# Optimization experiments

Hardware: AMD Instinct MI355X
Metric: run time of the kernel (lower is better)

## Reference

```python
import jax, jax.numpy as jnp
import numpy as np

EMBED = 256
HEADS = 8
LEVELS = 4
POINTS = 4
HD = EMBED // HEADS  # 32
SHAPES = [(100, 100), (50, 50), (25, 25), (13, 13)]  # (H, W) per level
NV = sum(h * w for h, w in SHAPES)  # 13294
BS = 2


def _lin_params(k, fan_in, fan_out):
    s = 1.0 / np.sqrt(fan_in)
    kw, kb = jax.random.split(k)
    W = jax.random.uniform(kw, (fan_in, fan_out), jnp.float32, -s, s)
    b = jax.random.uniform(kb, (fan_out,), jnp.float32, -s, s)
    return W, b


def setup_inputs():
    key = jax.random.key(0)
    ks = jax.random.split(key, 10)
    inp = {
        "query": jax.random.normal(ks[0], (BS, NV, EMBED), jnp.float32),
        "key": jax.random.normal(ks[1], (BS, NV, EMBED), jnp.float32),
        "value": jax.random.normal(ks[2], (BS, NV, EMBED), jnp.float32),
        "query_pos": jax.random.normal(ks[3], (BS, NV, EMBED), jnp.float32),
        "reference_points": jax.random.uniform(ks[4], (BS, NV, LEVELS, 2), jnp.float32),
        "spatial_shapes": jnp.array(SHAPES, jnp.int32),
        "level_start_index": jnp.array(np.cumsum([0] + [h * w for h, w in SHAPES[:-1]]), jnp.int32),
        "key_padding_mask": jnp.zeros((BS, NV), bool),
    }
    inp["W_value"], inp["b_value"] = _lin_params(ks[5], EMBED, EMBED)
    inp["W_off"], inp["b_off"] = _lin_params(ks[6], EMBED, HEADS * LEVELS * POINTS * 2)
    inp["W_attn"], inp["b_attn"] = _lin_params(ks[7], EMBED, HEADS * LEVELS * POINTS)
    inp["W_out"], inp["b_out"] = _lin_params(ks[8], EMBED, EMBED)
    inp["W_ffn"], inp["b_ffn"] = _lin_params(ks[9], EMBED, EMBED)
    return inp


def _bilinear(v, x, y, H, W):
    # v: (bs, heads, H*W, hd); x, y: (bs, heads, n) pixel coords (align_corners=False)
    # zero padding outside the feature map (matches torch grid_sample padding_mode='zeros')
    x0 = jnp.floor(x)
    y0 = jnp.floor(y)
    lx = x - x0
    ly = y - y0
    x0 = x0.astype(jnp.int32)
    y0 = y0.astype(jnp.int32)

    def g(xi, yi):
        valid = ((xi >= 0) & (xi < W) & (yi >= 0) & (yi < H)).astype(v.dtype)
        idx = jnp.clip(yi, 0, H - 1) * W + jnp.clip(xi, 0, W - 1)
        return jnp.take_along_axis(v, idx[..., None], axis=2) * valid[..., None]

    return (g(x0, y0) * ((1 - lx) * (1 - ly))[..., None]
            + g(x0 + 1, y0) * (lx * (1 - ly))[..., None]
            + g(x0, y0 + 1) * ((1 - lx) * ly)[..., None]
            + g(x0 + 1, y0 + 1) * (lx * ly)[..., None])


def _forward(query, key, value, query_pos, reference_points, shapes, starts,
             key_padding_mask, W_value, b_value, W_off, b_off, W_attn, b_attn,
             W_out, b_out, W_ffn, b_ffn):
    bs, nq, _ = query.shape
    identity = query  # residual taken BEFORE adding positional encoding (mmcv semantics)
    q = query + query_pos
    v = value @ W_value + b_value
    v = jnp.where(key_padding_mask[..., None], 0.0, v).reshape(bs, -1, HEADS, HD)
    off = (q @ W_off + b_off).reshape(bs, nq, HEADS, LEVELS, POINTS, 2)
    aw = jax.nn.softmax((q @ W_attn + b_attn).reshape(bs, nq, HEADS, LEVELS * POINTS), axis=-1)
    aw = aw.reshape(bs, nq, HEADS, LEVELS, POINTS)
    # offset normalizer is (W, H) per level
    wh = jnp.array([[w, h] for h, w in shapes], jnp.float32)
    loc = reference_points[:, :, None, :, None, :] + off / wh[None, None, None, :, None, :]
    out = jnp.zeros((bs, HEADS, nq, HD), q.dtype)
    for l, (H, W) in enumerate(shapes):
        s = starts[l]
        vl = v[:, s:s + H * W].transpose(0, 2, 1, 3)  # (bs, heads, H*W, hd)
        x = (loc[:, :, :, l, :, 0] * W - 0.5).transpose(0, 2, 1, 3).reshape(bs, HEADS, nq * POINTS)
        y = (loc[:, :, :, l, :, 1] * H - 0.5).transpose(0, 2, 1, 3).reshape(bs, HEADS, nq * POINTS)
        smp = _bilinear(vl, x, y, H, W).reshape(bs, HEADS, nq, POINTS, HD)
        wl = aw[:, :, :, l].transpose(0, 2, 1, 3)  # (bs, heads, nq, P)
        out = out + jnp.sum(smp * wl[..., None], axis=3)
    out = out.transpose(0, 2, 1, 3).reshape(bs, nq, EMBED)
    out = out @ W_out + b_out + identity
    return out @ W_ffn + b_ffn


def reference(query, key, value, query_pos, reference_points, spatial_shapes,
              level_start_index, key_padding_mask, W_value, b_value, W_off, b_off,
              W_attn, b_attn, W_out, b_out, W_ffn, b_ffn):
    # spatial shapes / level starts are structural metadata -> treat as static ints
    shapes = [tuple(int(x) for x in r) for r in np.asarray(spatial_shapes)]
    starts = [int(x) for x in np.asarray(level_start_index)]
    return _forward(query, key, value, query_pos, reference_points, shapes, starts,
                    key_padding_mask, W_value, b_value, W_off, b_off, W_attn, b_attn,
                    W_out, b_out, W_ffn, b_ffn)
```

## Files before the change

### kernel.cpp

```cpp
#include <hip/hip_runtime.h>
#include <hip/hip_bf16.h>
#include <math.h>

#define NQ 13294
#define NV 13294
#define M_ROWS (2*NQ)
#define MP 26624

typedef __attribute__((ext_vector_type(8))) short bf16x8;
typedef __attribute__((ext_vector_type(4))) float f32x4;
typedef __attribute__((ext_vector_type(2))) float f32x2;

__device__ __forceinline__ float4 ld4(const float* p){ return *(const float4*)p; }
__device__ __forceinline__ float bfu_lo(unsigned int u){ return __uint_as_float(u << 16); }
__device__ __forceinline__ float bfu_hi(unsigned int u){ return __uint_as_float(u & 0xffff0000u); }
__device__ __forceinline__ unsigned short f2bf(float f){
  unsigned int u = __float_as_uint(f);
  u += 0x7fffu + ((u >> 16) & 1u);
  return (unsigned short)(u >> 16);
}
__device__ __forceinline__ unsigned int pk2(float a, float b){
  return (unsigned int)f2bf(a) | ((unsigned int)f2bf(b) << 16);
}
__device__ __forceinline__ void gl_lds16(const unsigned short* g, unsigned short* l) {
  __builtin_amdgcn_global_load_lds(
      (const __attribute__((address_space(1))) unsigned int*)g,
      (__attribute__((address_space(3))) unsigned int*)l, 16, 0, 0);
}

__global__ __launch_bounds__(256) void prep_all(
    const float* __restrict__ value, const float* __restrict__ query,
    const float* __restrict__ qpos,
    unsigned short* __restrict__ val_bf, unsigned short* __restrict__ q_bf,
    unsigned short* __restrict__ q2_bf,
    const float* __restrict__ wv, const float* __restrict__ wo,
    const float* __restrict__ wa, const float* __restrict__ wu,
    const float* __restrict__ wf, unsigned short* __restrict__ wt,
    float* __restrict__ bias_c,
    const float* __restrict__ b_out, const float* __restrict__ b_ffn)
{
  if (blockIdx.x >= 2048) {
    const int n = threadIdx.x;
    float acc = b_ffn[n];
    #pragma unroll 8
    for (int k = 0; k < 256; ++k)
      acc = fmaf(b_out[k], wf[k * 256 + n], acc);
    bias_c[n] = acc;
    return;
  }

  const int total = MP * 64;
  for (int i = blockIdx.x * 256 + threadIdx.x; i < total; i += 2048 * 256) {
    const int e = i * 4;
    ushort4 a = make_ushort4(0,0,0,0), b = make_ushort4(0,0,0,0), c = make_ushort4(0,0,0,0);
    if (e < M_ROWS * 256) {
      float4 v4 = ld4(value + e);
      a = make_ushort4(f2bf(v4.x), f2bf(v4.y), f2bf(v4.z), f2bf(v4.w));
      float4 q4 = ld4(query + e);
      float4 p4 = ld4(qpos + e);
      b = make_ushort4(f2bf(q4.x+p4.x), f2bf(q4.y+p4.y), f2bf(q4.z+p4.z), f2bf(q4.w+p4.w));
      c = make_ushort4(f2bf(q4.x), f2bf(q4.y), f2bf(q4.z), f2bf(q4.w));
    }
    *(ushort4*)(val_bf + e) = a;
    *(ushort4*)(q_bf   + e) = b;
    *(ushort4*)(q2_bf  + e) = c;
  }
  for (int t = blockIdx.x * 256 + threadIdx.x; t < 294912; t += 2048 * 256) {
    if (t < 229376) {
      const float* src; int Nn; int base;
      if      (t < 65536)  { src = wv; Nn = 256; base = 0; }
      else if (t < 131072) { src = wo; Nn = 256; base = 65536; }
      else if (t < 163840) { src = wa; Nn = 128; base = 131072; }
      else                 { src = wf; Nn = 256; base = 163840; }
      const int local = t - base;
      const int n = local >> 8, k = local & 255;
      wt[t] = f2bf(src[k * Nn + n]);
    } else {
      const int local = t - 229376;
      wt[t] = f2bf(wu[local]);
    }
  }
}

__global__ __launch_bounds__(256) void gemm_voa2(
    const unsigned short* __restrict__ val_bf, const unsigned short* __restrict__ q_bf,
    const unsigned short* __restrict__ wv_t, const unsigned short* __restrict__ woa_t,
    const unsigned short* __restrict__ wf_t, const unsigned short* __restrict__ wu_bf,
    const float* __restrict__ b_value, const float* __restrict__ b_off,
    const float* __restrict__ b_attn,
    unsigned char* __restrict__ vbuf8, unsigned short* __restrict__ oa,
    unsigned short* __restrict__ wof_t)
{
  __shared__ unsigned short lds[32768];

  const int bx = blockIdx.x;
  const int mode = (bx < 1664) ? 0 : (bx < 4160) ? 1 : 2;
  const int lin  = (mode == 0) ? bx : (mode == 1) ? bx - 1664 : bx - 4160;
  const int nwg  = (mode == 0) ? 1664 : (mode == 1) ? 2496 : 16;
  const int ncol = (mode == 0) ? 4 : (mode == 1) ? 6 : 4;
  const unsigned short* A  = (mode == 0) ? val_bf : (mode == 1) ? q_bf : wf_t;
  const unsigned short* Bt = (mode == 0) ? wv_t : (mode == 1) ? woa_t : wu_bf;

  const int swz  = (lin & 7) * (nwg >> 3) + (lin >> 3);
  const int brow = (swz / ncol) * 64;
  const int bcol = (swz % ncol) * 64;

  const int tid  = threadIdx.x;
  const int wid  = tid >> 6, lane = tid & 63;
  const int wr   = wid >> 1, wc = wid & 1;
  const int fr   = lane & 15, fg = lane >> 4;

  {
    const int r0   = lane >> 3;
    const int slot = lane & 7;
    #pragma unroll
    for (int t = 0; t < 4; ++t) {
      #pragma unroll
      for (int c = 0; c < 2; ++c) {
        const int row = (wid * 2 + c) * 8 + r0;
        const int gsl = slot ^ (row & 7);
        gl_lds16(A  + (size_t)(brow + row) * 256 + t * 64 + (gsl << 3),
                 &lds[t * 4096 + (wid * 2 + c) * 512]);
        gl_lds16(Bt + (size_t)(bcol + row) * 256 + t * 64 + (gsl << 3),
                 &lds[16384 + t * 4096 + (wid * 2 + c) * 512]);
      }
    }
  }
  __syncthreads();

  f32x4 acc[2][2];
  #pragma unroll
  for (int m = 0; m < 2; ++m)
    #pragma unroll
    for (int n = 0; n < 2; ++n)
      acc[m][n] = (f32x4){0.f, 0.f, 0.f, 0.f};

  #pragma unroll
  for (int t = 0; t < 4; ++t) {
    const char* as = (const char*)&lds[t * 4096];
    const char* bs = (const char*)&lds[16384 + t * 4096];
    #pragma unroll
    for (int kk = 0; kk < 2; ++kk) {
      const int kb = kk * 64 + fg * 16;
      bf16x8 af[2], bfv[2];
      #pragma unroll
      for (int m = 0; m < 2; ++m) {
        const int r = wr * 32 + m * 16 + fr;
        af[m] = *(const bf16x8*)(as + r * 128 + (kb ^ ((r & 7) << 4)));
      }
      #pragma unroll
      for (int n = 0; n < 2; ++n) {
        const int r = wc * 32 + n * 16 + fr;
        bfv[n] = *(const bf16x8*)(bs + r * 128 + (kb ^ ((r & 7) << 4)));
      }
      #pragma unroll
      for (int m = 0; m < 2; ++m)
        #pragma unroll
        for (int n = 0; n < 2; ++n)
          acc[m][n] = __builtin_amdgcn_mfma_f32_16x16x32_bf16(af[m], bfv[n], acc[m][n], 0, 0, 0);
    }
  }

  __syncthreads();
  float* csh = (float*)lds;
  const int c0 = bcol + wc * 32 + fr;
  const int c1 = c0 + 16;
  float bn0 = 0.f, bn1 = 0.f;
  if (mode == 0) { bn0 = b_value[c0]; bn1 = b_value[c1]; }
  else if (mode == 1) {
    bn0 = (c0 < 256) ? b_off[c0] : b_attn[c0 - 256];
    bn1 = (c1 < 256) ? b_off[c1] : b_attn[c1 - 256];
  }
  #pragma unroll
  for (int m = 0; m < 2; ++m)
    #pragma unroll
    for (int j = 0; j < 4; ++j) {
      const int row = wr * 32 + m * 16 + fg * 4 + j;
      csh[row * 64 + wc * 32 + fr]      = acc[m][0][j] + bn0;
      csh[row * 64 + wc * 32 + 16 + fr] = acc[m][1][j] + bn1;
    }
  __syncthreads();
  #pragma unroll
  for (int i = 0; i < 4; ++i) {
    const int rl = i * 16 + (tid >> 4);
    const int gr = brow + rl;
    if (gr >= M_ROWS) continue;
    const int c4 = (tid & 15) * 4;
    float4 v = *(const float4*)&csh[rl * 64 + c4];
    if (mode == 0) {
      const int head = (bcol + c4) >> 5;
      const int ch   = c4 & 31;
      int r = 0;
      r = __builtin_amdgcn_cvt_pk_fp8_f32(v.x, v.y, r, 0);
      r = __builtin_amdgcn_cvt_pk_fp8_f32(v.z, v.w, r, 1);
      *(int*)&vbuf8[((size_t)head * M_ROWS + gr) * 32 + ch] = r;
    } else if (mode == 1) {
      ushort4 pk = make_ushort4(f2bf(v.x), f2bf(v.y), f2bf(v.z), f2bf(v.w));
      *(ushort4*)&oa[(size_t)gr * 384 + bcol + c4] = pk;
    } else {
      ushort4 pk = make_ushort4(f2bf(v.x), f2bf(v.y), f2bf(v.z), f2bf(v.w));
      *(ushort4*)&wof_t[(size_t)gr * 256 + bcol + c4] = pk;
    }
  }
}

__global__ __launch_bounds__(256) void gemm_final(
    const unsigned short* __restrict__ A1, const unsigned short* __restrict__ B1,
    const unsigned short* __restrict__ A2, const unsigned short* __restrict__ B2,
    const float* __restrict__ bias_c, float* __restrict__ C)
{
  __shared__ unsigned short lds[32768];

  const int nwg = 1664;
  const int lin = blockIdx.x;
  const int swz = (lin & 7) * (nwg >> 3) + (lin >> 3);
  const int brow = (swz >> 2) * 64;
  const int bcol = (swz & 3) * 64;

  const int tid  = threadIdx.x;
  const int wid  = tid >> 6, lane = tid & 63;
  const int wr   = wid >> 1, wc = wid & 1;
  const int fr   = lane & 15, fg = lane >> 4;

  auto stage = [&](const unsigned short* A, const unsigned short* Bt) {
    const int r0   = lane >> 3;
    const int slot = lane & 7;
    #pragma unroll
    for (int t = 0; t < 4; ++t) {
      #pragma unroll
      for (int c = 0; c < 2; ++c) {
        const int row = (wid * 2 + c) * 8 + r0;
        const int gsl = slot ^ (row & 7);
        gl_lds16(A  + (size_t)(brow + row) * 256 + t * 64 + (gsl << 3),
                 &lds[t * 4096 + (wid * 2 + c) * 512]);
        gl_lds16(Bt + (size_t)(bcol + row) * 256 + t * 64 + (gsl << 3),
                 &lds[16384 + t * 4096 + (wid * 2 + c) * 512]);
      }
    }
  };

  f32x4 acc[2][2];
  #pragma unroll
  for (int m = 0; m < 2; ++m)
    #pragma unroll
    for (int n = 0; n < 2; ++n)
      acc[m][n] = (f32x4){0.f, 0.f, 0.f, 0.f};

  auto compute = [&]() {
    #pragma unroll
    for (int t = 0; t < 4; ++t) {
      const char* as = (const char*)&lds[t * 4096];
      const char* bs = (const char*)&lds[16384 + t * 4096];
      #pragma unroll
      for (int kk = 0; kk < 2; ++kk) {
        const int kb = kk * 64 + fg * 16;
        bf16x8 af[2], bfv[2];
        #pragma unroll
        for (int m = 0; m < 2; ++m) {
          const int r = wr * 32 + m * 16 + fr;
          af[m] = *(const bf16x8*)(as + r * 128 + (kb ^ ((r & 7) << 4)));
        }
        #pragma unroll
        for (int n = 0; n < 2; ++n) {
          const int r = wc * 32 + n * 16 + fr;
          bfv[n] = *(const bf16x8*)(bs + r * 128 + (kb ^ ((r & 7) << 4)));
        }
        #pragma unroll
        for (int m = 0; m < 2; ++m)
          #pragma unroll
          for (int n = 0; n < 2; ++n)
            acc[m][n] = __builtin_amdgcn_mfma_f32_16x16x32_bf16(af[m], bfv[n], acc[m][n], 0, 0, 0);
      }
    }
  };

  stage(A1, B1);
  __syncthreads();
  compute();
  __syncthreads();
  stage(A2, B2);
  __syncthreads();
  compute();

  __syncthreads();
  float* csh = (float*)lds;
  const int c0 = bcol + wc * 32 + fr;
  const int c1 = c0 + 16;
  const float bn0 = bias_c[c0];
  const float bn1 = bias_c[c1];
  #pragma unroll
  for (int m = 0; m < 2; ++m)
    #pragma unroll
    for (int j = 0; j < 4; ++j) {
      const int row = wr * 32 + m * 16 + fg * 4 + j;
      csh[row * 64 + wc * 32 + fr]      = acc[m][0][j] + bn0;
      csh[row * 64 + wc * 32 + 16 + fr] = acc[m][1][j] + bn1;
    }
  __syncthreads();
  #pragma unroll
  for (int i = 0; i < 4; ++i) {
    const int rl = i * 16 + (tid >> 4);
    const int gr = brow + rl;
    if (gr >= M_ROWS) continue;
    const int c4 = (tid & 15) * 4;
    *(float4*)&C[(size_t)gr * 256 + bcol + c4] = *(const float4*)&csh[rl * 64 + c4];
  }
}

__global__ __launch_bounds__(256) void msda7(
    const unsigned char* __restrict__ v, const unsigned short* __restrict__ oa,
    const float* __restrict__ ref, unsigned short* __restrict__ attout)
{
  constexpr int LW[4] = {100, 50, 25, 13};
  constexpr int LS[4] = {0, 10000, 12500, 13125};

  __shared__ int2   sidx[64][17];
  __shared__ float4 swt [64][17];

  const int bid   = blockIdx.x;
  const int h     = bid & 7;
  const int chunk = bid >> 3;
  const int tid   = threadIdx.x;
  const int q     = tid >> 2;
  const int c     = tid & 3;
  const int bq    = chunk * 64 + q;
  const bool active = bq < M_ROWS;
  const int b     = (bq >= NQ) ? 1 : 0;

  if (active) {
    const int l = c;
    const int W = LW[l];
    const float fD = (float)W;
    const unsigned short* oarow = oa + (size_t)bq * 384;

    uint2 lg = *(const uint2*)(oarow + 256 + h * 16 + l * 4);
    float g0 = bfu_lo(lg.x), g1 = bfu_hi(lg.x), g2 = bfu_lo(lg.y), g3 = bfu_hi(lg.y);
    float mx = fmaxf(fmaxf(g0, g1), fmaxf(g2, g3));
    mx = fmaxf(mx, __shfl_xor(mx, 1));
    mx = fmaxf(mx, __shfl_xor(mx, 2));
    float e0 = __expf(g0-mx), e1 = __expf(g1-mx), e2 = __expf(g2-mx), e3 = __expf(g3-mx);
    float s = e0 + e1 + e2 + e3;
    s += __shfl_xor(s, 1);
    s += __shfl_xor(s, 2);
    const float inv = 1.f / s;
    const float ee[4] = {e0*inv, e1*inv, e2*inv, e3*inv};

    uint4 ov = *(const uint4*)(oarow + h * 32 + l * 8);
    const float oxy[8] = {bfu_lo(ov.x), bfu_hi(ov.x), bfu_lo(ov.y), bfu_hi(ov.y),
                          bfu_lo(ov.z), bfu_hi(ov.z), bfu_lo(ov.w), bfu_hi(ov.w)};
    const float rx = ref[(size_t)bq * 8 + l * 2];
    const float ry = ref[(size_t)bq * 8 + l * 2 + 1];
    const int rowbase = b * NV + LS[l];

    #pragma unroll
    for (int j = 0; j < 4; ++j) {
      const float x = fmaf(rx, fD, oxy[2*j])   - 0.5f;
      const float y = fmaf(ry, fD, oxy[2*j+1]) - 0.5f;
      const float x0f = floorf(x), y0f = floorf(y);
      const float lx = x - x0f, ly = y - y0f;
      const int x0 = (int)x0f, y0 = (int)y0f;
      const int y1 = y0 + 1;
      const int xbase = min(max(x0, 0), W - 2);
      const float wx0 = 1.f - lx, wx1 = lx;
      const float we0 = (x0 == xbase     ? wx0 : 0.f) + (x0 == xbase - 1 ? wx1 : 0.f);
      const float we1 = (x0 == xbase + 1 ? wx0 : 0.f) + (x0 == xbase     ? wx1 : 0.f);
      const int cy0 = min(max(y0, 0), W - 1), cy1 = min(max(y1, 0), W - 1);
      const float wy0 = (y0 >= 0 && y0 < W) ? (1.f - ly) : 0.f;
      const float wy1 = (y1 >= 0 && y1 < W) ? ly : 0.f;
      const float wt = ee[j];
      const int p = l * 4 + j;
      sidx[q][p] = make_int2((rowbase + cy0 * W + xbase) * 32,
                             (rowbase + cy1 * W + xbase) * 32);
      swt[q][p] = make_float4(wt * wy0 * we0, wt * wy0 * we1,
                              wt * wy1 * we0, wt * wy1 * we1);
    }
  }
  __syncthreads();

  if (active) {
    const unsigned char* vb = v + (size_t)h * M_ROWS * 32 + c * 16;
    const int el = c >> 1;
    f32x2 acc2[8];
    #pragma unroll
    for (int k = 0; k < 8; ++k) acc2[k] = (f32x2){0.f, 0.f};
    #pragma unroll
    for (int p = 0; p < 16; ++p) {
      const int2   ix = sidx[q][p];
      const float4 w4 = swt[q][p];
      uint4 r0 = *(const uint4*)(vb + ix.x);
      uint4 r1 = *(const uint4*)(vb + ix.y);
      const float wa = el ? w4.y : w4.x;
      const float wb = el ? w4.w : w4.z;
      const f32x2 wav = (f32x2){wa, wa};
      const f32x2 wbv = (f32x2){wb, wb};
      acc2[0] = wav * __builtin_amdgcn_cvt_pk_f32_fp8(r0.x, 0) + acc2[0];
      acc2[1] = wav * __builtin_amdgcn_cvt_pk_f32_fp8(r0.x, 1) + acc2[1];
      acc2[2] = wav * __builtin_amdgcn_cvt_pk_f32_fp8(r0.y, 0) + acc2[2];
      acc2[3] = wav * __builtin_amdgcn_cvt_pk_f32_fp8(r0.y, 1) + acc2[3];
      acc2[4] = wav * __builtin_amdgcn_cvt_pk_f32_fp8(r0.z, 0) + acc2[4];
      acc2[5] = wav * __builtin_amdgcn_cvt_pk_f32_fp8(r0.z, 1) + acc2[5];
      acc2[6] = wav * __builtin_amdgcn_cvt_pk_f32_fp8(r0.w, 0) + acc2[6];
      acc2[7] = wav * __builtin_amdgcn_cvt_pk_f32_fp8(r0.w, 1) + acc2[7];
      acc2[0] = wbv * __builtin_amdgcn_cvt_pk_f32_fp8(r1.x, 0) + acc2[0];
      acc2[1] = wbv * __builtin_amdgcn_cvt_pk_f32_fp8(r1.x, 1) + acc2[1];
      acc2[2] = wbv * __builtin_amdgcn_cvt_pk_f32_fp8(r1.y, 0) + acc2[2];
      acc2[3] = wbv * __builtin_amdgcn_cvt_pk_f32_fp8(r1.y, 1) + acc2[3];
      acc2[4] = wbv * __builtin_amdgcn_cvt_pk_f32_fp8(r1.z, 0) + acc2[4];
      acc2[5] = wbv * __builtin_amdgcn_cvt_pk_f32_fp8(r1.z, 1) + acc2[5];
      acc2[6] = wbv * __builtin_amdgcn_cvt_pk_f32_fp8(r1.w, 0) + acc2[6];
      acc2[7] = wbv * __builtin_amdgcn_cvt_pk_f32_fp8(r1.w, 1) + acc2[7];
    }
    #pragma unroll
    for (int k = 0; k < 8; ++k) {
      acc2[k][0] += __shfl_xor(acc2[k][0], 2);
      acc2[k][1] += __shfl_xor(acc2[k][1], 2);
    }
    if (c < 2) {
      uint4 pkA, pkB;
      pkA.x = pk2(acc2[0][0], acc2[0][1]);
      pkA.y = pk2(acc2[1][0], acc2[1][1]);
      pkA.z = pk2(acc2[2][0], acc2[2][1]);
      pkA.w = pk2(acc2[3][0], acc2[3][1]);
      pkB.x = pk2(acc2[4][0], acc2[4][1]);
      pkB.y = pk2(acc2[5][0], acc2[5][1]);
      pkB.z = pk2(acc2[6][0], acc2[6][1]);
      pkB.w = pk2(acc2[7][0], acc2[7][1]);
      unsigned short* dst = attout + (size_t)bq * 256 + h * 32 + c * 16;
      *(uint4*)dst = pkA;
      *(uint4*)(dst + 8) = pkB;
    }
  }
}

extern "C" void kernel_launch(void* const* d_in, const int* in_sizes, int n_in,
                              void* d_out, int out_size, void* d_ws, size_t ws_size,
                              hipStream_t stream) {
  const float* query  = (const float*)d_in[0];
  const float* value  = (const float*)d_in[2];
  const float* qpos   = (const float*)d_in[3];
  const float* refpts = (const float*)d_in[4];
  const float* W_value = (const float*)d_in[8];
  const float* b_value = (const float*)d_in[9];
  const float* W_off   = (const float*)d_in[10];
  const float* b_off   = (const float*)d_in[11];
  const float* W_attn  = (const float*)d_in[12];
  const float* b_attn  = (const float*)d_in[13];
  const float* W_out   = (const float*)d_in[14];
  const float* b_out   = (const float*)d_in[15];
  const float* W_ffn   = (const float*)d_in[16];
  const float* b_ffn   = (const float*)d_in[17];
  float* out = (float*)d_out;

  unsigned short* oa    = (unsigned short*)d_ws;
  unsigned char*  vbuf8 = (unsigned char*)(oa + (size_t)MP * 384);
  unsigned short* AB1   = (unsigned short*)(vbuf8 + (size_t)8 * M_ROWS * 32);
  unsigned short* QB    = AB1 + (size_t)MP * 256;
  unsigned short* Q2B   = QB + (size_t)MP * 256;
  unsigned short* wts   = Q2B + (size_t)MP * 256;
  unsigned short* wv_t  = wts;
  unsigned short* woa_t = wts + 65536;
  unsigned short* wf_t  = wts + 163840;
  unsigned short* wu_bf = wts + 229376;
  unsigned short* wof_t = wts + 294912;
  float*          bias_c = (float*)(wof_t + 65536);

  const dim3 blk(256);

  prep_all<<<dim3(2049), blk, 0, stream>>>(value, query, qpos, AB1, QB, Q2B,
      W_value, W_off, W_attn, W_out, W_ffn, wts, bias_c, b_out, b_ffn);

  gemm_voa2<<<dim3(1664 + 2496 + 16), blk, 0, stream>>>(
      AB1, QB, wv_t, woa_t, wf_t, wu_bf, b_value, b_off, b_attn, vbuf8, oa, wof_t);

  msda7<<<dim3(8 * 416), blk, 0, stream>>>(vbuf8, oa, refpts, AB1);

  gemm_final<<<dim3(1664), blk, 0, stream>>>(AB1, wof_t, Q2B, wf_t, bias_c, out);
}
```

Baseline: 109.5 us.

## Fuse fp32-to-bf16 activation conversion into GEMM LDS staging, drop prep pass

Removes the pass that converted value, query and query+pos to bf16 copies in workspace. The GEMMs now stage fp32 rows straight into LDS and convert them to bf16 while building the MFMA fragments. The query+pos input is handled as two accumulated passes (query, then qpos) using linearity, and the final GEMM reads fp32 query directly. The weight prep shrinks to a small kernel. This cuts the write and re-read of three bf16 activation copies, at the cost of twice the LDS traffic per A tile, extra pack instructions, doubled MFMA work for the offset/attention GEMM, and separate bf16 rounding of query and pos.

```diff
diff --git a/kernel.cpp b/kernel.cpp
--- a/kernel.cpp
+++ b/kernel.cpp
@@ -11,7 +11,6 @@
 typedef __attribute__((ext_vector_type(4))) float f32x4;
 typedef __attribute__((ext_vector_type(2))) float f32x2;
 
-__device__ __forceinline__ float4 ld4(const float* p){ return *(const float4*)p; }
 __device__ __forceinline__ float bfu_lo(unsigned int u){ return __uint_as_float(u << 16); }
 __device__ __forceinline__ float bfu_hi(unsigned int u){ return __uint_as_float(u & 0xffff0000u); }
 __device__ __forceinline__ unsigned short f2bf(float f){
@@ -22,68 +21,48 @@
 __device__ __forceinline__ unsigned int pk2(float a, float b){
   return (unsigned int)f2bf(a) | ((unsigned int)f2bf(b) << 16);
 }
-__device__ __forceinline__ void gl_lds16(const unsigned short* g, unsigned short* l) {
+__device__ __forceinline__ void gl_lds16(const void* g, unsigned short* l) {
   __builtin_amdgcn_global_load_lds(
       (const __attribute__((address_space(1))) unsigned int*)g,
       (__attribute__((address_space(3))) unsigned int*)l, 16, 0, 0);
 }
 
-__global__ __launch_bounds__(256) void prep_all(
-    const float* __restrict__ value, const float* __restrict__ query,
-    const float* __restrict__ qpos,
-    unsigned short* __restrict__ val_bf, unsigned short* __restrict__ q_bf,
-    unsigned short* __restrict__ q2_bf,
+__global__ __launch_bounds__(256) void prep_w(
     const float* __restrict__ wv, const float* __restrict__ wo,
     const float* __restrict__ wa, const float* __restrict__ wu,
     const float* __restrict__ wf, unsigned short* __restrict__ wt,
     float* __restrict__ bias_c,
     const float* __restrict__ b_out, const float* __restrict__ b_ffn)
 {
-  if (blockIdx.x >= 2048) {
+  const int bx = blockIdx.x;
+  if (bx < 64) {
+    for (int t = bx * 256 + threadIdx.x; t < 294912; t += 64 * 256) {
+      if (t < 229376) {
+        const float* src; int Nn; int base;
+        if      (t < 65536)  { src = wv; Nn = 256; base = 0; }
+        else if (t < 131072) { src = wo; Nn = 256; base = 65536; }
+        else if (t < 163840) { src = wa; Nn = 128; base = 131072; }
+        else                 { src = wf; Nn = 256; base = 163840; }
+        const int local = t - base;
+        const int n = local >> 8, k = local & 255;
+        wt[t] = f2bf(src[k * Nn + n]);
+      } else {
+        wt[t] = f2bf(wu[t - 229376]);
+      }
+    }
+  } else {
     const int n = threadIdx.x;
     float acc = b_ffn[n];
     #pragma unroll 8
     for (int k = 0; k < 256; ++k)
       acc = fmaf(b_out[k], wf[k * 256 + n], acc);
     bias_c[n] = acc;
-    return;
-  }
-
-  const int total = MP * 64;
-  for (int i = blockIdx.x * 256 + threadIdx.x; i < total; i += 2048 * 256) {
-    const int e = i * 4;
-    ushort4 a = make_ushort4(0,0,0,0), b = make_ushort4(0,0,0,0), c = make_ushort4(0,0,0,0);
-    if (e < M_ROWS * 256) {
-      float4 v4 = ld4(value + e);
-      a = make_ushort4(f2bf(v4.x), f2bf(v4.y), f2bf(v4.z), f2bf(v4.w));
-      float4 q4 = ld4(query + e);
-      float4 p4 = ld4(qpos + e);
-      b = make_ushort4(f2bf(q4.x+p4.x), f2bf(q4.y+p4.y), f2bf(q4.z+p4.z), f2bf(q4.w+p4.w));
-      c = make_ushort4(f2bf(q4.x), f2bf(q4.y), f2bf(q4.z), f2bf(q4.w));
-    }
-    *(ushort4*)(val_bf + e) = a;
-    *(ushort4*)(q_bf   + e) = b;
-    *(ushort4*)(q2_bf  + e) = c;
-  }
-  for (int t = blockIdx.x * 256 + threadIdx.x; t < 294912; t += 2048 * 256) {
-    if (t < 229376) {
-      const float* src; int Nn; int base;
-      if      (t < 65536)  { src = wv; Nn = 256; base = 0; }
-      else if (t < 131072) { src = wo; Nn = 256; base = 65536; }
-      else if (t < 163840) { src = wa; Nn = 128; base = 131072; }
-      else                 { src = wf; Nn = 256; base = 163840; }
-      const int local = t - base;
-      const int n = local >> 8, k = local & 255;
-      wt[t] = f2bf(src[k * Nn + n]);
-    } else {
-      const int local = t - 229376;
-      wt[t] = f2bf(wu[local]);
-    }
-  }
-}
-
-__global__ __launch_bounds__(256) void gemm_voa2(
-    const unsigned short* __restrict__ val_bf, const unsigned short* __restrict__ q_bf,
+  }
+}
+
+__global__ __launch_bounds__(256) void gemm_voa3(
+    const float* __restrict__ value, const float* __restrict__ query,
+    const float* __restrict__ qpos,
     const unsigned short* __restrict__ wv_t, const unsigned short* __restrict__ woa_t,
     const unsigned short* __restrict__ wf_t, const unsigned short* __restrict__ wu_bf,
     const float* __restrict__ b_value, const float* __restrict__ b_off,
@@ -98,7 +77,6 @@
   const int lin  = (mode == 0) ? bx : (mode == 1) ? bx - 1664 : bx - 4160;
   const int nwg  = (mode == 0) ? 1664 : (mode == 1) ? 2496 : 16;
   const int ncol = (mode == 0) ? 4 : (mode == 1) ? 6 : 4;
-  const unsigned short* A  = (mode == 0) ? val_bf : (mode == 1) ? q_bf : wf_t;
   const unsigned short* Bt = (mode == 0) ? wv_t : (mode == 1) ? woa_t : wu_bf;
 
   const int swz  = (lin & 7) * (nwg >> 3) + (lin >> 3);
@@ -111,22 +89,17 @@
   const int fr   = lane & 15, fg = lane >> 4;
 
   {
-    const int r0   = lane >> 3;
-    const int slot = lane & 7;
-    #pragma unroll
-    for (int t = 0; t < 4; ++t) {
+    const int r0 = lane >> 3, slot = lane & 7;
+    #pragma unroll
+    for (int t = 0; t < 4; ++t)
       #pragma unroll
       for (int c = 0; c < 2; ++c) {
         const int row = (wid * 2 + c) * 8 + r0;
         const int gsl = slot ^ (row & 7);
-        gl_lds16(A  + (size_t)(brow + row) * 256 + t * 64 + (gsl << 3),
-                 &lds[t * 4096 + (wid * 2 + c) * 512]);
         gl_lds16(Bt + (size_t)(bcol + row) * 256 + t * 64 + (gsl << 3),
                  &lds[16384 + t * 4096 + (wid * 2 + c) * 512]);
       }
-    }
-  }
-  __syncthreads();
+  }
 
   f32x4 acc[2][2];
   #pragma unroll
@@ -135,29 +108,103 @@
     for (int n = 0; n < 2; ++n)
       acc[m][n] = (f32x4){0.f, 0.f, 0.f, 0.f};
 
-  #pragma unroll
-  for (int t = 0; t < 4; ++t) {
-    const char* as = (const char*)&lds[t * 4096];
-    const char* bs = (const char*)&lds[16384 + t * 4096];
-    #pragma unroll
-    for (int kk = 0; kk < 2; ++kk) {
-      const int kb = kk * 64 + fg * 16;
-      bf16x8 af[2], bfv[2];
-      #pragma unroll
-      for (int m = 0; m < 2; ++m) {
-        const int r = wr * 32 + m * 16 + fr;
-        af[m] = *(const bf16x8*)(as + r * 128 + (kb ^ ((r & 7) << 4)));
-      }
-      #pragma unroll
-      for (int n = 0; n < 2; ++n) {
-        const int r = wc * 32 + n * 16 + fr;
-        bfv[n] = *(const bf16x8*)(bs + r * 128 + (kb ^ ((r & 7) << 4)));
-      }
-      #pragma unroll
-      for (int m = 0; m < 2; ++m)
-        #pragma unroll
-        for (int n = 0; n < 2; ++n)
-          acc[m][n] = __builtin_amdgcn_mfma_f32_16x16x32_bf16(af[m], bfv[n], acc[m][n], 0, 0, 0);
+  if (mode == 2) {
+    {
+      const int r0 = lane >> 3, slot = lane & 7;
+      #pragma unroll
+      for (int t = 0; t < 4; ++t)
+        #pragma unroll
+        for (int c = 0; c < 2; ++c) {
+          const int row = (wid * 2 + c) * 8 + r0;
+          const int gsl = slot ^ (row & 7);
+          gl_lds16(wf_t + (size_t)(brow + row) * 256 + t * 64 + (gsl << 3),
+                   &lds[t * 4096 + (wid * 2 + c) * 512]);
+        }
+    }
+    __syncthreads();
+    #pragma unroll
+    for (int t = 0; t < 4; ++t) {
+      const char* as = (const char*)&lds[t * 4096];
+      const char* bs = (const char*)&lds[16384 + t * 4096];
+      #pragma unroll
+      for (int kk = 0; kk < 2; ++kk) {
+        const int kb = kk * 64 + fg * 16;
+        bf16x8 af[2], bfv[2];
+        #pragma unroll
+        for (int m = 0; m < 2; ++m) {
+          const int r = wr * 32 + m * 16 + fr;
+          af[m] = *(const bf16x8*)(as + r * 128 + (kb ^ ((r & 7) << 4)));
+        }
+        #pragma unroll
+        for (int n = 0; n < 2; ++n) {
+          const int r = wc * 32 + n * 16 + fr;
+          bfv[n] = *(const bf16x8*)(bs + r * 128 + (kb ^ ((r & 7) << 4)));
+        }
+        #pragma unroll
+        for (int m = 0; m < 2; ++m)
+          #pragma unroll
+          for (int n = 0; n < 2; ++n)
+            acc[m][n] = __builtin_amdgcn_mfma_f32_16x16x32_bf16(af[m], bfv[n], acc[m][n], 0, 0, 0);
+      }
+    }
+  } else {
+    const int npass = (mode == 0) ? 1 : 2;
+    for (int ps = 0; ps < npass; ++ps) {
+      const float* S = (mode == 0) ? value : (ps == 0 ? query : qpos);
+      for (int half = 0; half < 2; ++half) {
+        if (ps | half) __syncthreads();
+        {
+          const int rl = lane >> 4;
+          const int sl = lane & 15;
+          #pragma unroll
+          for (int t2 = 0; t2 < 2; ++t2) {
+            const int kt = half * 2 + t2;
+            #pragma unroll
+            for (int i = 0; i < 4; ++i) {
+              const int c = wid * 4 + i;
+              const int row = c * 4 + rl;
+              const int gr = min(brow + row, M_ROWS - 1);
+              const int gsl = sl ^ (row & 7);
+              gl_lds16(S + (size_t)gr * 256 + kt * 64 + gsl * 4,
+                       &lds[t2 * 8192 + c * 512]);
+            }
+          }
+        }
+        __syncthreads();
+        #pragma unroll
+        for (int t2 = 0; t2 < 2; ++t2) {
+          const int kt = half * 2 + t2;
+          const char* as = (const char*)&lds[t2 * 8192];
+          const char* bs = (const char*)&lds[16384 + kt * 4096];
+          #pragma unroll
+          for (int kk = 0; kk < 2; ++kk) {
+            const int s  = kk * 8 + fg * 2;
+            const int kb = kk * 64 + fg * 16;
+            bf16x8 af[2], bfv[2];
+            #pragma unroll
+            for (int m = 0; m < 2; ++m) {
+              const int r  = wr * 32 + m * 16 + fr;
+              const int e7 = r & 7;
+              f32x4 a0 = *(const f32x4*)(as + r * 256 + ((s       ^ e7) << 4));
+              f32x4 a1 = *(const f32x4*)(as + r * 256 + (((s + 1) ^ e7) << 4));
+              union { unsigned int u[4]; bf16x8 h; } cv;
+              cv.u[0] = pk2(a0[0], a0[1]); cv.u[1] = pk2(a0[2], a0[3]);
+              cv.u[2] = pk2(a1[0], a1[1]); cv.u[3] = pk2(a1[2], a1[3]);
+              af[m] = cv.h;
+            }
+            #pragma unroll
+            for (int n = 0; n < 2; ++n) {
+              const int r = wc * 32 + n * 16 + fr;
+              bfv[n] = *(const bf16x8*)(bs + r * 128 + (kb ^ ((r & 7) << 4)));
+            }
+            #pragma unroll
+            for (int m = 0; m < 2; ++m)
+              #pragma unroll
+              for (int n = 0; n < 2; ++n)
+                acc[m][n] = __builtin_amdgcn_mfma_f32_16x16x32_bf16(af[m], bfv[n], acc[m][n], 0, 0, 0);
+          }
+        }
+      }
     }
   }
 
@@ -184,7 +231,7 @@
   for (int i = 0; i < 4; ++i) {
     const int rl = i * 16 + (tid >> 4);
     const int gr = brow + rl;
-    if (gr >= M_ROWS) continue;
+    if (gr >= M_ROWS && mode != 2) continue;
     const int c4 = (tid & 15) * 4;
     float4 v = *(const float4*)&csh[rl * 64 + c4];
     if (mode == 0) {
@@ -204,9 +251,9 @@
   }
 }
 
-__global__ __launch_bounds__(256) void gemm_final(
-    const unsigned short* __restrict__ A1, const unsigned short* __restrict__ B1,
-    const unsigned short* __restrict__ A2, const unsigned short* __restrict__ B2,
+__global__ __launch_bounds__(256) void gemm_final2(
+    const unsigned short* __restrict__ attout, const unsigned short* __restrict__ wof_t,
+    const float* __restrict__ query, const unsigned short* __restrict__ wf_t,
     const float* __restrict__ bias_c, float* __restrict__ C)
 {
   __shared__ unsigned short lds[32768];
@@ -222,21 +269,17 @@
   const int wr   = wid >> 1, wc = wid & 1;
   const int fr   = lane & 15, fg = lane >> 4;
 
-  auto stage = [&](const unsigned short* A, const unsigned short* Bt) {
-    const int r0   = lane >> 3;
-    const int slot = lane & 7;
-    #pragma unroll
-    for (int t = 0; t < 4; ++t) {
+  auto stage_b = [&](const unsigned short* Bt) {
+    const int r0 = lane >> 3, slot = lane & 7;
+    #pragma unroll
+    for (int t = 0; t < 4; ++t)
       #pragma unroll
       for (int c = 0; c < 2; ++c) {
         const int row = (wid * 2 + c) * 8 + r0;
         const int gsl = slot ^ (row & 7);
-        gl_lds16(A  + (size_t)(brow + row) * 256 + t * 64 + (gsl << 3),
-                 &lds[t * 4096 + (wid * 2 + c) * 512]);
         gl_lds16(Bt + (size_t)(bcol + row) * 256 + t * 64 + (gsl << 3),
                  &lds[16384 + t * 4096 + (wid * 2 + c) * 512]);
       }
-    }
   };
 
   f32x4 acc[2][2];
@@ -246,19 +289,87 @@
     for (int n = 0; n < 2; ++n)
       acc[m][n] = (f32x4){0.f, 0.f, 0.f, 0.f};
 
-  auto compute = [&]() {
-    #pragma unroll
-    for (int t = 0; t < 4; ++t) {
-      const char* as = (const char*)&lds[t * 4096];
-      const char* bs = (const char*)&lds[16384 + t * 4096];
+  stage_b(wof_t);
+  {
+    const int r0 = lane >> 3, slot = lane & 7;
+    #pragma unroll
+    for (int t = 0; t < 4; ++t)
+      #pragma unroll
+      for (int c = 0; c < 2; ++c) {
+        const int row = (wid * 2 + c) * 8 + r0;
+        const int gsl = slot ^ (row & 7);
+        gl_lds16(attout + (size_t)(brow + row) * 256 + t * 64 + (gsl << 3),
+                 &lds[t * 4096 + (wid * 2 + c) * 512]);
+      }
+  }
+  __syncthreads();
+  #pragma unroll
+  for (int t = 0; t < 4; ++t) {
+    const char* as = (const char*)&lds[t * 4096];
+    const char* bs = (const char*)&lds[16384 + t * 4096];
+    #pragma unroll
+    for (int kk = 0; kk < 2; ++kk) {
+      const int kb = kk * 64 + fg * 16;
+      bf16x8 af[2], bfv[2];
+      #pragma unroll
+      for (int m = 0; m < 2; ++m) {
+        const int r = wr * 32 + m * 16 + fr;
+        af[m] = *(const bf16x8*)(as + r * 128 + (kb ^ ((r & 7) << 4)));
+      }
+      #pragma unroll
+      for (int n = 0; n < 2; ++n) {
+        const int r = wc * 32 + n * 16 + fr;
+        bfv[n] = *(const bf16x8*)(bs + r * 128 + (kb ^ ((r & 7) << 4)));
+      }
+      #pragma unroll
+      for (int m = 0; m < 2; ++m)
+        #pragma unroll
+        for (int n = 0; n < 2; ++n)
+          acc[m][n] = __builtin_amdgcn_mfma_f32_16x16x32_bf16(af[m], bfv[n], acc[m][n], 0, 0, 0);
+    }
+  }
+
+  for (int half = 0; half < 2; ++half) {
+    __syncthreads();
+    if (half == 0) stage_b(wf_t);
+    {
+      const int rl = lane >> 4;
+      const int sl = lane & 15;
+      #pragma unroll
+      for (int t2 = 0; t2 < 2; ++t2) {
+        const int kt = half * 2 + t2;
+        #pragma unroll
+        for (int i = 0; i < 4; ++i) {
+          const int c = wid * 4 + i;
+          const int row = c * 4 + rl;
+          const int gr = min(brow + row, M_ROWS - 1);
+          const int gsl = sl ^ (row & 7);
+          gl_lds16(query + (size_t)gr * 256 + kt * 64 + gsl * 4,
+                   &lds[t2 * 8192 + c * 512]);
+        }
+      }
+    }
+    __syncthreads();
+    #pragma unroll
+    for (int t2 = 0; t2 < 2; ++t2) {
+      const int kt = half * 2 + t2;
+      const char* as = (const char*)&lds[t2 * 8192];
+      const char* bs = (const char*)&lds[16384 + kt * 4096];
       #pragma unroll
       for (int kk = 0; kk < 2; ++kk) {
+        const int s  = kk * 8 + fg * 2;
         const int kb = kk * 64 + fg * 16;
         bf16x8 af[2], bfv[2];
         #pragma unroll
         for (int m = 0; m < 2; ++m) {
-          const int r = wr * 32 + m * 16 + fr;
-          af[m] = *(const bf16x8*)(as + r * 128 + (kb ^ ((r & 7) << 4)));
+          const int r  = wr * 32 + m * 16 + fr;
+          const int e7 = r & 7;
+          f32x4 a0 = *(const f32x4*)(as + r * 256 + ((s       ^ e7) << 4));
+          f32x4 a1 = *(const f32x4*)(as + r * 256 + (((s + 1) ^ e7) << 4));
+          union { unsigned int u[4]; bf16x8 h; } cv;
+          cv.u[0] = pk2(a0[0], a0[1]); cv.u[1] = pk2(a0[2], a0[3]);
+          cv.u[2] = pk2(a1[0], a1[1]); cv.u[3] = pk2(a1[2], a1[3]);
+          af[m] = cv.h;
         }
         #pragma unroll
         for (int n = 0; n < 2; ++n) {
@@ -272,15 +383,7 @@
             acc[m][n] = __builtin_amdgcn_mfma_f32_16x16x32_bf16(af[m], bfv[n], acc[m][n], 0, 0, 0);
       }
     }
-  };
-
-  stage(A1, B1);
-  __syncthreads();
-  compute();
-  __syncthreads();
-  stage(A2, B2);
-  __syncthreads();
-  compute();
+  }
 
   __syncthreads();
   float* csh = (float*)lds;
@@ -454,9 +557,7 @@
   unsigned short* oa    = (unsigned short*)d_ws;
   unsigned char*  vbuf8 = (unsigned char*)(oa + (size_t)MP * 384);
   unsigned short* AB1   = (unsigned short*)(vbuf8 + (size_t)8 * M_ROWS * 32);
-  unsigned short* QB    = AB1 + (size_t)MP * 256;
-  unsigned short* Q2B   = QB + (size_t)MP * 256;
-  unsigned short* wts   = Q2B + (size_t)MP * 256;
+  unsigned short* wts   = AB1 + (size_t)MP * 256;
   unsigned short* wv_t  = wts;
   unsigned short* woa_t = wts + 65536;
   unsigned short* wf_t  = wts + 163840;
@@ -466,13 +567,14 @@
 
   const dim3 blk(256);
 
-  prep_all<<<dim3(2049), blk, 0, stream>>>(value, query, qpos, AB1, QB, Q2B,
-      W_value, W_off, W_attn, W_out, W_ffn, wts, bias_c, b_out, b_ffn);
-
-  gemm_voa2<<<dim3(1664 + 2496 + 16), blk, 0, stream>>>(
-      AB1, QB, wv_t, woa_t, wf_t, wu_bf, b_value, b_off, b_attn, vbuf8, oa, wof_t);
+  prep_w<<<dim3(65), blk, 0, stream>>>(W_value, W_off, W_attn, W_out, W_ffn,
+                                       wts, bias_c, b_out, b_ffn);
+
+  gemm_voa3<<<dim3(1664 + 2496 + 16), blk, 0, stream>>>(
+      value, query, qpos, wv_t, woa_t, wf_t, wu_bf,
+      b_value, b_off, b_attn, vbuf8, oa, wof_t);
 
   msda7<<<dim3(8 * 416), blk, 0, stream>>>(vbuf8, oa, refpts, AB1);
 
-  gemm_final<<<dim3(1664), blk, 0, stream>>>(AB1, wof_t, Q2B, wf_t, bias_c, out);
-}
+  gemm_final2<<<dim3(1664), blk, 0, stream>>>(AB1, wof_t, query, wf_t, bias_c, out);
+}
```

Result: slower. 124.3 us (+13.5%).
